# Kernel optimization log

Measured on AMD Instinct MI355X. Metric: run time of the kernel, lower is better.

The kernel has to match this reference:

```python
import jax, jax.numpy as jnp
import numpy as np

B, X, Y, C, H = 16, 64, 64, 256, 8
N = X * Y
EPS_LN, EPS_BN = 1e-6, 1e-5

def _conv3x3(x, w):
    return jax.lax.conv_general_dilated(x, w, (1, 1), 'SAME', dimension_numbers=('NCHW', 'OIHW', 'NCHW'))

def _bn(x, g, b, m, v):
    # eval-mode BatchNorm2d with running stats
    s = g / jnp.sqrt(v + EPS_BN)
    return x * s[None, :, None, None] + (b - m * s)[None, :, None, None]

def _ln(x, g, b):
    mu = jnp.mean(x, -1, keepdims=True)
    var = jnp.mean((x - mu) ** 2, -1, keepdims=True)
    return (x - mu) * jax.lax.rsqrt(var + EPS_LN) * g + b

def _rotate_half(x):
    x1, x2 = jnp.split(x, 2, axis=-1)
    return jnp.concatenate([-x2, x1], axis=-1)

def _rope(t, f):
    return t * jnp.cos(f) + _rotate_half(t) * jnp.sin(f)

def setup_inputs() -> dict:
    key = jax.random.key(0)
    ks = jax.random.split(key, 9)
    p = {}
    p['input'] = jax.random.normal(ks[0], (B, X, Y), jnp.float32)
    p['freq_x'] = jax.random.normal(ks[1], (B, N, C // 2), jnp.float32)
    p['freq_y'] = jax.random.normal(ks[2], (B, N, C // 2), jnp.float32)
    p['conv1_w'] = jax.random.normal(ks[3], (C, 1, 3, 3), jnp.float32) * 0.1
    p['conv2_w'] = jax.random.normal(ks[4], (C, C, 3, 3), jnp.float32) * 0.02
    for nm in ('bn1', 'bn2'):
        p[nm + '_g'] = jnp.ones((C,), jnp.float32)
        p[nm + '_b'] = jnp.zeros((C,), jnp.float32)
        p[nm + '_m'] = jnp.zeros((C,), jnp.float32)
        p[nm + '_v'] = jnp.ones((C,), jnp.float32)
    p['ln1_g'] = jnp.ones((C,), jnp.float32); p['ln1_b'] = jnp.zeros((C,), jnp.float32)
    p['ln2_g'] = jnp.ones((C,), jnp.float32); p['ln2_b'] = jnp.zeros((C,), jnp.float32)
    p['qkv_w'] = jax.random.normal(ks[5], (3 * C, C), jnp.float32) * 0.02
    p['out_w'] = jax.random.normal(ks[6], (C, C), jnp.float32) * 0.02
    p['out_b'] = jnp.zeros((C,), jnp.float32)
    p['mlp_w1'] = jax.random.normal(ks[7], (C, C), jnp.float32) * 0.02
    p['mlp_b1'] = jnp.zeros((C,), jnp.float32)
    p['mlp_w2'] = jax.random.normal(ks[8], (C, C), jnp.float32) * 0.02
    p['mlp_b2'] = jnp.zeros((C,), jnp.float32)
    return p

def reference(input, freq_x, freq_y, conv1_w, conv2_w, bn1_g, bn1_b, bn1_m, bn1_v, bn2_g, bn2_b, bn2_m, bn2_v, ln1_g, ln1_b, ln2_g, ln2_b, qkv_w, out_w, out_b, mlp_w1, mlp_b1, mlp_w2, mlp_b2):
    x4 = input[:, None]  # [B,1,X,Y]
    out = jax.nn.relu(_bn(_conv3x3(x4, conv1_w), bn1_g, bn1_b, bn1_m, bn1_v))
    out = jax.nn.relu(_bn(_conv3x3(out, conv2_w), bn2_g, bn2_b, bn2_m, bn2_v))
    feat = jax.nn.relu(x4 + out)  # broadcast residual add, [B,C,X,Y]
    inp = feat.transpose(0, 2, 3, 1).reshape(B, N, C)  # 'b h x y -> b (x y) h'
    # --- attention/MLP branch (computed as in source; its result is discarded) ---
    x = _ln(inp, ln1_g, ln1_b)
    tx, ty = x[..., :C // 2], x[..., C // 2:]
    x = jnp.concatenate([_rope(tx, freq_x), _rope(ty, freq_y)], -1)
    qkv = x @ qkv_w.T  # [B,N,3C]
    q, k, v = jnp.split(qkv, 3, -1)
    def _heads(t):
        return t.reshape(B, N, H, C // H).transpose(0, 2, 1, 3)  # [B,H,N,Dh]
    q, k, v = _heads(q), _heads(k), _heads(v)
    q = jax.nn.softmax(q, -1) * ((C // H) ** -0.5)
    k = jax.nn.softmax(k, -2)
    ctx = jnp.einsum('bhnd,bhne->bhde', k, v)   # [B,H,Dh,Dh]
    o = jnp.einsum('bhnd,bhde->bhne', q, ctx)   # [B,H,N,Dh]
    o = o.transpose(0, 2, 1, 3).reshape(B, N, C) @ out_w.T + out_b
    x = o + inp
    y = _ln(x, ln2_g, ln2_b)
    y = jax.nn.gelu(y @ mlp_w1.T + mlp_b1, approximate=False) @ mlp_w2.T + mlp_b2
    x = x + y
    # source module returns `input` (the post-stem tokens), not `x`
    return inp
```

## Files before the change

### kernel.cpp

```cpp
#include <hip/hip_runtime.h>
#include <hip/hip_bf16.h>

#define BB 16
#define XY 64
#define CC 256
#define PD 66

typedef __attribute__((ext_vector_type(8))) short short8;
typedef __attribute__((ext_vector_type(4))) float f32x4;
typedef __hip_bfloat16 bf16;

__device__ __forceinline__ void glds16(const void* g, void* l) {
  __builtin_amdgcn_global_load_lds(
      (const __attribute__((address_space(1))) void*)g,
      (__attribute__((address_space(3))) void*)l, 16, 0, 0);
}

__global__ __launch_bounds__(256) void k_conv1(
    const float* __restrict__ in,
    const float* __restrict__ w1,
    const float* __restrict__ g, const float* __restrict__ bbias,
    const float* __restrict__ m, const float* __restrict__ v,
    bf16* __restrict__ act)
{
  int blk = blockIdx.x;
  int b = blk / PD, hp = blk % PD;
  int c = threadIdx.x;
  bf16* actrow = act + (size_t)(b * PD + hp) * PD * CC;
  if (hp == 0 || hp == PD - 1) {
    for (int wp = 0; wp < PD; ++wp) actrow[wp * CC + c] = __float2bfloat16(0.f);
    return;
  }
  __shared__ float inrow[3][PD];
  int h = hp - 1;
  for (int t = threadIdx.x; t < 3 * PD; t += 256) {
    int r = t / PD, x = t % PD;
    int hr = h - 1 + r, wr = x - 1;
    inrow[r][x] = (hr >= 0 && hr < XY && wr >= 0 && wr < XY)
                      ? in[(b * XY + hr) * XY + wr] : 0.f;
  }
  __syncthreads();
  float w[9];
#pragma unroll
  for (int t = 0; t < 9; ++t) w[t] = w1[c * 9 + t];
  float s  = g[c] * rsqrtf(v[c] + 1e-5f);
  float tt = bbias[c] - m[c] * s;
  actrow[c] = __float2bfloat16(0.f);
  actrow[(PD - 1) * CC + c] = __float2bfloat16(0.f);
  for (int wp = 1; wp <= XY; ++wp) {
    float o = 0.f;
#pragma unroll
    for (int dy = 0; dy < 3; ++dy)
#pragma unroll
      for (int dx = 0; dx < 3; ++dx)
        o = fmaf(inrow[dy][wp - 1 + dx], w[dy * 3 + dx], o);
    actrow[wp * CC + c] = __float2bfloat16(fmaxf(fmaf(o, s, tt), 0.f));
  }
}

__global__ __launch_bounds__(256) void k_wb(
    const float* __restrict__ w2,
    const float* __restrict__ g, const float* __restrict__ v,
    bf16* __restrict__ Wb)
{
  int e = blockIdx.x * 256 + threadIdx.x;
  int j   = e & 7;
  int co  = (e >> 3) & 255;
  int qq  = (e >> 11) & 3;
  int c   = (e >> 13) & 7;
  int tap = e >> 16;
  int ci = c * 32 + qq * 8 + j;
  float s = g[co] * rsqrtf(v[co] + 1e-5f);
  Wb[e] = __float2bfloat16(w2[((size_t)co * CC + ci) * 9 + tap] * s);
}

__global__ __launch_bounds__(256, 3) void k_conv2(
    const bf16* __restrict__ act,
    const bf16* __restrict__ Wb,
    const float* __restrict__ in,
    const float* __restrict__ g2, const float* __restrict__ b2,
    const float* __restrict__ m2, const float* __restrict__ v2,
    float* __restrict__ out)
{
  __shared__ alignas(16) bf16 As[3 * 4 * PD * 8];
  __shared__ alignas(16) bf16 Ws[4 * CC * 8];
  __shared__ float inrow[XY];

  int blk = blockIdx.x;
  int b = blk >> 6, h = blk & 63;
  int tid = threadIdx.x;
  int lane = tid & 63, wv = tid >> 6;
  int m = lane & 15, q = lane >> 4;

  f32x4 acc[4][4];
#pragma unroll
  for (int i = 0; i < 4; ++i)
#pragma unroll
    for (int j = 0; j < 4; ++j) acc[i][j] = f32x4{0.f, 0.f, 0.f, 0.f};

  if (tid < XY) inrow[tid] = in[(b * XY + h) * XY + tid];

  const bf16* actbase = act + (size_t)(b * PD + h) * PD * CC;

  for (int c = 0; c < 8; ++c) {
    for (int tap = 0; tap < 9; ++tap) {
      const bf16* wsrc = Wb + (size_t)(tap * 8 + c) * 8192;
#pragma unroll
      for (int i = 0; i < 4; ++i) {
        int seg = wv * 4 + i;
        glds16((const char*)wsrc + seg * 1024 + lane * 16,
               (char*)Ws + seg * 1024);
      }
      if (tap == 0) {
        for (int idx = tid; idx < 792; idx += 256) {
          int qq = idx & 3, p = idx >> 2;
          int r = p / PD, wp = p % PD;
          short8 val = *(const short8*)(actbase + (size_t)(r * PD + wp) * CC + c * 32 + qq * 8);
          *(short8*)&As[((r * 4 + qq) * PD + wp) * 8] = val;
        }
      }
      __syncthreads();

      int dy = tap / 3, dx = tap % 3;
      short8 af[4], bfr[4];
#pragma unroll
      for (int mt = 0; mt < 4; ++mt)
        af[mt] = *(const short8*)&As[((dy * 4 + q) * PD + mt * 16 + m + dx) * 8];
#pragma unroll
      for (int nt = 0; nt < 4; ++nt)
        bfr[nt] = *(const short8*)&Ws[(q * CC + wv * 64 + nt * 16 + m) * 8];
#pragma unroll
      for (int mt = 0; mt < 4; ++mt)
#pragma unroll
        for (int nt = 0; nt < 4; ++nt)
          acc[mt][nt] = __builtin_amdgcn_mfma_f32_16x16x32_bf16(
              af[mt], bfr[nt], acc[mt][nt], 0, 0, 0);
      __syncthreads();
    }
  }

  float t2[4];
#pragma unroll
  for (int nt = 0; nt < 4; ++nt) {
    int co = wv * 64 + nt * 16 + m;
    float s2 = g2[co] * rsqrtf(v2[co] + 1e-5f);
    t2[nt] = b2[co] - m2[co] * s2;
  }
  float* ob = out + (size_t)(b * XY + h) * XY * CC;
#pragma unroll
  for (int mt = 0; mt < 4; ++mt)
#pragma unroll
    for (int r = 0; r < 4; ++r) {
      int wp = mt * 16 + q * 4 + r;
      float iv = inrow[wp];
#pragma unroll
      for (int nt = 0; nt < 4; ++nt) {
        int co = wv * 64 + nt * 16 + m;
        float val = fmaxf(acc[mt][nt][r] + t2[nt], 0.f);
        ob[(size_t)wp * CC + co] = fmaxf(iv + val, 0.f);
      }
    }
}

extern "C" void kernel_launch(void* const* d_in, const int* in_sizes, int n_in,
                              void* d_out, int out_size, void* d_ws, size_t ws_size,
                              hipStream_t stream) {
  const float* in_   = (const float*)d_in[0];
  const float* w1    = (const float*)d_in[3];
  const float* w2    = (const float*)d_in[4];
  const float* bn1_g = (const float*)d_in[5];
  const float* bn1_b = (const float*)d_in[6];
  const float* bn1_m = (const float*)d_in[7];
  const float* bn1_v = (const float*)d_in[8];
  const float* bn2_g = (const float*)d_in[9];
  const float* bn2_b = (const float*)d_in[10];
  const float* bn2_m = (const float*)d_in[11];
  const float* bn2_v = (const float*)d_in[12];
  float* out = (float*)d_out;

  bf16* act = (bf16*)d_ws;
  bf16* Wb  = act + (size_t)BB * PD * PD * CC;

  k_conv1<<<BB * PD, 256, 0, stream>>>(in_, w1, bn1_g, bn1_b, bn1_m, bn1_v, act);
  k_wb<<<(9 * CC * CC) / 256, 256, 0, stream>>>(w2, bn2_g, bn2_v, Wb);
  k_conv2<<<BB * XY, 256, 0, stream>>>(act, Wb, in_, bn2_g, bn2_b, bn2_m, bn2_v, out);
}
```

Before: 102.8 us.

## Double-buffer conv2 weights, compute two output rows per block, swizzle LDS

The conv2 kernel now computes two output rows per block, so each 4-row activation slab serves 8 M-tiles and weight-tile loads are amortized over twice the work. Weight tiles are double-buffered in LDS: the next tap's weights are prefetched with global_load_lds while the current MFMAs run, with manual vmcnt waits and raw barriers in place of __syncthreads. The activation tile gets a padded stride and the weight layout an XOR swizzle, both meant to cut LDS bank conflicts. Blocks are remapped across XCDs, and conv1 writes packed bf16 pairs. The changes raise register pressure (occupancy hint goes from 3 to 2) and halve the grid to 512 blocks.

```diff
diff --git a/kernel.cpp b/kernel.cpp
--- a/kernel.cpp
+++ b/kernel.cpp
@@ -5,10 +5,12 @@
 #define XY 64
 #define CC 256
 #define PD 66
+#define AST 67
 
 typedef __attribute__((ext_vector_type(8))) short short8;
 typedef __attribute__((ext_vector_type(4))) float f32x4;
 typedef __hip_bfloat16 bf16;
+typedef __hip_bfloat162 bf16x2;
 
 __device__ __forceinline__ void glds16(const void* g, void* l) {
   __builtin_amdgcn_global_load_lds(
@@ -25,36 +27,45 @@
 {
   int blk = blockIdx.x;
   int b = blk / PD, hp = blk % PD;
-  int c = threadIdx.x;
-  bf16* actrow = act + (size_t)(b * PD + hp) * PD * CC;
+  int tid = threadIdx.x;
+  bf16x2* actrow = (bf16x2*)(act + (size_t)(b * PD + hp) * PD * CC);
+  bf16x2 z; z.x = __float2bfloat16(0.f); z.y = z.x;
   if (hp == 0 || hp == PD - 1) {
-    for (int wp = 0; wp < PD; ++wp) actrow[wp * CC + c] = __float2bfloat16(0.f);
+    for (int i = tid; i < PD * 128; i += 256) actrow[i] = z;
     return;
   }
   __shared__ float inrow[3][PD];
   int h = hp - 1;
-  for (int t = threadIdx.x; t < 3 * PD; t += 256) {
+  for (int t = tid; t < 3 * PD; t += 256) {
     int r = t / PD, x = t % PD;
     int hr = h - 1 + r, wr = x - 1;
     inrow[r][x] = (hr >= 0 && hr < XY && wr >= 0 && wr < XY)
                       ? in[(b * XY + hr) * XY + wr] : 0.f;
   }
   __syncthreads();
-  float w[9];
-#pragma unroll
-  for (int t = 0; t < 9; ++t) w[t] = w1[c * 9 + t];
-  float s  = g[c] * rsqrtf(v[c] + 1e-5f);
-  float tt = bbias[c] - m[c] * s;
-  actrow[c] = __float2bfloat16(0.f);
-  actrow[(PD - 1) * CC + c] = __float2bfloat16(0.f);
-  for (int wp = 1; wp <= XY; ++wp) {
-    float o = 0.f;
+  int cp = tid & 127, half = tid >> 7;
+  int c0 = cp * 2;
+  float wa[9], wb_[9];
+#pragma unroll
+  for (int t = 0; t < 9; ++t) { wa[t] = w1[c0 * 9 + t]; wb_[t] = w1[(c0 + 1) * 9 + t]; }
+  float s0 = g[c0] * rsqrtf(v[c0] + 1e-5f),     t0 = bbias[c0] - m[c0] * s0;
+  float s1 = g[c0+1] * rsqrtf(v[c0+1] + 1e-5f), t1 = bbias[c0+1] - m[c0+1] * s1;
+  actrow[(half ? (PD - 1) : 0) * 128 + cp] = z;
+  for (int i = 0; i < 32; ++i) {
+    int wp = half * 32 + 1 + i;
+    float o0 = 0.f, o1 = 0.f;
 #pragma unroll
     for (int dy = 0; dy < 3; ++dy)
 #pragma unroll
-      for (int dx = 0; dx < 3; ++dx)
-        o = fmaf(inrow[dy][wp - 1 + dx], w[dy * 3 + dx], o);
-    actrow[wp * CC + c] = __float2bfloat16(fmaxf(fmaf(o, s, tt), 0.f));
+      for (int dx = 0; dx < 3; ++dx) {
+        float iv = inrow[dy][wp - 1 + dx];
+        o0 = fmaf(iv, wa[dy * 3 + dx], o0);
+        o1 = fmaf(iv, wb_[dy * 3 + dx], o1);
+      }
+    bf16x2 rr;
+    rr.x = __float2bfloat16(fmaxf(fmaf(o0, s0, t0), 0.f));
+    rr.y = __float2bfloat16(fmaxf(fmaf(o1, s1, t1), 0.f));
+    actrow[wp * 128 + cp] = rr;
   }
 }
 
@@ -65,16 +76,17 @@
 {
   int e = blockIdx.x * 256 + threadIdx.x;
   int j   = e & 7;
-  int co  = (e >> 3) & 255;
-  int qq  = (e >> 11) & 3;
-  int c   = (e >> 13) & 7;
+  int P   = (e >> 3) & 1023;
+  int cc  = (e >> 13) & 7;
   int tap = e >> 16;
-  int ci = c * 32 + qq * 8 + j;
+  int L = P ^ (((P >> 8) & 3) << 1);
+  int qq = L >> 8, co = L & 255;
+  int ci = cc * 32 + qq * 8 + j;
   float s = g[co] * rsqrtf(v[co] + 1e-5f);
   Wb[e] = __float2bfloat16(w2[((size_t)co * CC + ci) * 9 + tap] * s);
 }
 
-__global__ __launch_bounds__(256, 3) void k_conv2(
+__global__ __launch_bounds__(256, 2) void k_conv2(
     const bf16* __restrict__ act,
     const bf16* __restrict__ Wb,
     const float* __restrict__ in,
@@ -82,84 +94,137 @@
     const float* __restrict__ m2, const float* __restrict__ v2,
     float* __restrict__ out)
 {
-  __shared__ alignas(16) bf16 As[3 * 4 * PD * 8];
-  __shared__ alignas(16) bf16 Ws[4 * CC * 8];
-  __shared__ float inrow[XY];
-
-  int blk = blockIdx.x;
-  int b = blk >> 6, h = blk & 63;
+  __shared__ alignas(16) bf16 As[16 * AST * 8];
+  __shared__ alignas(16) bf16 Ws[2][1024 * 8];
+  __shared__ float inrow[128];
+
+  int gg = blockIdx.x;
+  int blk = (gg & 7) * 64 + (gg >> 3);
+  int b = blk >> 5, h0 = (blk & 31) * 2;
+
   int tid = threadIdx.x;
   int lane = tid & 63, wv = tid >> 6;
   int m = lane & 15, q = lane >> 4;
 
-  f32x4 acc[4][4];
-#pragma unroll
-  for (int i = 0; i < 4; ++i)
+  f32x4 acc[8][4];
+#pragma unroll
+  for (int i = 0; i < 8; ++i)
 #pragma unroll
     for (int j = 0; j < 4; ++j) acc[i][j] = f32x4{0.f, 0.f, 0.f, 0.f};
 
-  if (tid < XY) inrow[tid] = in[(b * XY + h) * XY + tid];
-
-  const bf16* actbase = act + (size_t)(b * PD + h) * PD * CC;
-
+  if (tid < 128) inrow[tid] = in[(b * XY + h0 + (tid >> 6)) * XY + (tid & 63)];
+  __syncthreads();
+
+  const bf16* actbase = act + ((size_t)(b * PD) + h0) * PD * CC;
+
+#pragma unroll
+  for (int i = 0; i < 4; ++i) {
+    int seg = wv * 4 + i;
+    glds16((const char*)Wb + seg * 1024 + lane * 16, (char*)&Ws[0][0] + seg * 1024);
+  }
+
+  int kt = 0;
   for (int c = 0; c < 8; ++c) {
-    for (int tap = 0; tap < 9; ++tap) {
-      const bf16* wsrc = Wb + (size_t)(tap * 8 + c) * 8192;
-#pragma unroll
-      for (int i = 0; i < 4; ++i) {
-        int seg = wv * 4 + i;
-        glds16((const char*)wsrc + seg * 1024 + lane * 16,
-               (char*)Ws + seg * 1024);
-      }
+    for (int tap = 0; tap < 9; ++tap, ++kt) {
+      int cur = kt & 1;
+      __builtin_amdgcn_s_barrier();
+      short8 areg[4], aregR;
       if (tap == 0) {
-        for (int idx = tid; idx < 792; idx += 256) {
-          int qq = idx & 3, p = idx >> 2;
-          int r = p / PD, wp = p % PD;
-          short8 val = *(const short8*)(actbase + (size_t)(r * PD + wp) * CC + c * 32 + qq * 8);
-          *(short8*)&As[((r * 4 + qq) * PD + wp) * 8] = val;
-        }
-      }
-      __syncthreads();
+#pragma unroll
+        for (int i = 0; i < 4; ++i) {
+          int idx = tid + i * 256;
+          int qq = idx & 3, p = idx >> 2;
+          int r = p / PD, wp = p % PD;
+          areg[i] = *(const short8*)(actbase + ((size_t)(r * PD + wp)) * CC + c * 32 + qq * 8);
+        }
+        if (tid < 32) {
+          int idx = 1024 + tid;
+          int qq = idx & 3, p = idx >> 2;
+          int r = p / PD, wp = p % PD;
+          aregR = *(const short8*)(actbase + ((size_t)(r * PD + wp)) * CC + c * 32 + qq * 8);
+        }
+        __builtin_amdgcn_sched_barrier(0);
+      }
+      if (kt + 1 < 72) {
+        int tap1 = (tap == 8) ? 0 : tap + 1;
+        int c1   = (tap == 8) ? c + 1 : c;
+        const bf16* wsrc = Wb + (size_t)(tap1 * 8 + c1) * 8192;
+#pragma unroll
+        for (int i = 0; i < 4; ++i) {
+          int seg = wv * 4 + i;
+          glds16((const char*)wsrc + seg * 1024 + lane * 16,
+                 (char*)&Ws[cur ^ 1][0] + seg * 1024);
+        }
+        asm volatile("s_waitcnt vmcnt(4)" ::: "memory");
+      } else {
+        asm volatile("s_waitcnt vmcnt(0)" ::: "memory");
+      }
+      if (tap == 0) {
+#pragma unroll
+        for (int i = 0; i < 4; ++i) {
+          int idx = tid + i * 256;
+          int qq = idx & 3, p = idx >> 2;
+          int r = p / PD, wp = p % PD;
+          *(short8*)&As[((r * 4 + qq) * AST + wp) * 8] = areg[i];
+        }
+        if (tid < 32) {
+          int idx = 1024 + tid;
+          int qq = idx & 3, p = idx >> 2;
+          int r = p / PD, wp = p % PD;
+          *(short8*)&As[((r * 4 + qq) * AST + wp) * 8] = aregR;
+        }
+        asm volatile("s_waitcnt lgkmcnt(0)" ::: "memory");
+      }
+      __builtin_amdgcn_s_barrier();
+      __builtin_amdgcn_sched_barrier(0);
 
       int dy = tap / 3, dx = tap % 3;
-      short8 af[4], bfr[4];
-#pragma unroll
-      for (int mt = 0; mt < 4; ++mt)
-        af[mt] = *(const short8*)&As[((dy * 4 + q) * PD + mt * 16 + m + dx) * 8];
-#pragma unroll
-      for (int nt = 0; nt < 4; ++nt)
-        bfr[nt] = *(const short8*)&Ws[(q * CC + wv * 64 + nt * 16 + m) * 8];
-#pragma unroll
-      for (int mt = 0; mt < 4; ++mt)
+      short8 af[8], bfr[4];
+#pragma unroll
+      for (int mt = 0; mt < 8; ++mt) {
+        int rg = (mt >> 2) + dy;
+        int wp = (mt & 3) * 16 + m + dx;
+        af[mt] = *(const short8*)&As[((rg * 4 + q) * AST + wp) * 8];
+      }
+#pragma unroll
+      for (int nt = 0; nt < 4; ++nt) {
+        int Lc = (q << 8) + (wv << 6) + nt * 16 + m;
+        bfr[nt] = *(const short8*)&Ws[cur][(Lc ^ (q << 1)) * 8];
+      }
+      __builtin_amdgcn_s_setprio(1);
+#pragma unroll
+      for (int mt = 0; mt < 8; ++mt)
 #pragma unroll
         for (int nt = 0; nt < 4; ++nt)
           acc[mt][nt] = __builtin_amdgcn_mfma_f32_16x16x32_bf16(
               af[mt], bfr[nt], acc[mt][nt], 0, 0, 0);
-      __syncthreads();
+      __builtin_amdgcn_s_setprio(0);
     }
   }
 
   float t2[4];
 #pragma unroll
   for (int nt = 0; nt < 4; ++nt) {
-    int co = wv * 64 + nt * 16 + m;
+    int co = (wv << 6) + nt * 16 + m;
     float s2 = g2[co] * rsqrtf(v2[co] + 1e-5f);
     t2[nt] = b2[co] - m2[co] * s2;
   }
-  float* ob = out + (size_t)(b * XY + h) * XY * CC;
-#pragma unroll
-  for (int mt = 0; mt < 4; ++mt)
+#pragma unroll
+  for (int mt = 0; mt < 8; ++mt) {
+    int r_out = mt >> 2;
+    float* ob = out + ((size_t)(b * XY + h0 + r_out)) * XY * CC;
 #pragma unroll
     for (int r = 0; r < 4; ++r) {
-      int wp = mt * 16 + q * 4 + r;
-      float iv = inrow[wp];
+      int wp = (mt & 3) * 16 + q * 4 + r;
+      float iv = inrow[r_out * 64 + wp];
 #pragma unroll
       for (int nt = 0; nt < 4; ++nt) {
-        int co = wv * 64 + nt * 16 + m;
+        int co = (wv << 6) + nt * 16 + m;
         float val = fmaxf(acc[mt][nt][r] + t2[nt], 0.f);
         ob[(size_t)wp * CC + co] = fmaxf(iv + val, 0.f);
       }
     }
+  }
 }
 
 extern "C" void kernel_launch(void* const* d_in, const int* in_sizes, int n_in,
@@ -183,5 +248,5 @@
 
   k_conv1<<<BB * PD, 256, 0, stream>>>(in_, w1, bn1_g, bn1_b, bn1_m, bn1_v, act);
   k_wb<<<(9 * CC * CC) / 256, 256, 0, stream>>>(w2, bn2_g, bn2_v, Wb);
-  k_conv2<<<BB * XY, 256, 0, stream>>>(act, Wb, in_, bn2_g, bn2_b, bn2_m, bn2_v, out);
-}
+  k_conv2<<<512, 256, 0, stream>>>(act, Wb, in_, bn2_g, bn2_b, bn2_m, bn2_v, out);
+}
```

After: 98.88 us. -3.9%, faster.
